# Kernel tuning notes

Measured on AMD Instinct MI355X. Metric: run time of the kernel, lower is better.

Reference implementation:

```python
import jax, jax.numpy as jnp
import numpy as np

OUT_F, IN_F = 11008, 4096
GROUP_SIZE = 128
NUM_GROUPS = IN_F // GROUP_SIZE  # 32


def setup_inputs() -> dict:
    key = jax.random.key(0)
    k1, k2, k3, k4 = jax.random.split(key, 4)
    x = jax.random.normal(k1, (2, 2048, IN_F), dtype=jnp.float32)
    # signed 4-bit RTN codes in [-8, 7]
    qweight = jax.random.randint(k2, (OUT_F, IN_F), 0, 16, dtype=jnp.int32) - 8
    # per-group scales (out_features, in_features // group_size)
    scales = jax.random.uniform(k3, (OUT_F, NUM_GROUPS), dtype=jnp.float32) * 0.02 + 1e-3
    bias = jax.random.normal(k4, (OUT_F,), dtype=jnp.float32) * 0.01
    return {"x": x, "qweight": qweight, "scales": scales, "bias": bias}


def reference(x, qweight, scales, bias):
    # RTN dequant: w[o, i] = qweight[o, i] * scales[o, i // group_size]
    w = (qweight.astype(x.dtype).reshape(OUT_F, NUM_GROUPS, GROUP_SIZE)
         * scales[:, :, None]).reshape(OUT_F, IN_F)
    # y = x @ w.T + bias  -> [batch, seq, out_features]
    return jnp.einsum('bsi,oi->bso', x, w) + bias
```

## Files before the change

### kernel.cpp

```cpp
#include <hip/hip_runtime.h>

#define OUT_F 11008
#define IN_F  4096
#define M_TOT 4096
#define BM    256
#define BN    256
#define BK    64
#define NKT   (IN_F / BK)
#define TM_N  (M_TOT / BM)
#define TN_N  (OUT_F / BN)
#define NWG   (TM_N * TN_N)

typedef __bf16 bf16;
typedef __attribute__((ext_vector_type(8))) __bf16 bf16x8;
typedef __attribute__((ext_vector_type(4))) float  floatx4;

#define GLD_LDS16(g, l) __builtin_amdgcn_global_load_lds(                      \
    (const __attribute__((address_space(1))) unsigned int*)(g),                \
    (__attribute__((address_space(3))) unsigned int*)(l), 16, 0, 0)

__global__ __launch_bounds__(256) void dequant_w_kernel(
    const int* __restrict__ qw, const float* __restrict__ sc,
    bf16* __restrict__ w) {
  const int idx  = blockIdx.x * 256 + threadIdx.x;
  const int o    = idx >> 9;
  const int iv   = idx & 511;
  const float s  = sc[o * (IN_F / 128) + (iv >> 4)];
  const int base = idx * 8;
  const int4* p  = (const int4*)(qw + base);
  const int4 q0  = p[0];
  const int4 q1  = p[1];
  bf16x8 v;
  v[0] = (bf16)((float)q0.x * s);
  v[1] = (bf16)((float)q0.y * s);
  v[2] = (bf16)((float)q0.z * s);
  v[3] = (bf16)((float)q0.w * s);
  v[4] = (bf16)((float)q1.x * s);
  v[5] = (bf16)((float)q1.y * s);
  v[6] = (bf16)((float)q1.z * s);
  v[7] = (bf16)((float)q1.w * s);
  *(bf16x8*)(w + base) = v;
}

__global__ __launch_bounds__(256) void cast_x_kernel(
    const float* __restrict__ x, bf16* __restrict__ xb) {
  const int idx  = blockIdx.x * 256 + threadIdx.x;
  const int base = idx * 8;
  const float4* p = (const float4*)(x + base);
  const float4 a = p[0];
  const float4 b = p[1];
  bf16x8 v;
  v[0] = (bf16)a.x; v[1] = (bf16)a.y; v[2] = (bf16)a.z; v[3] = (bf16)a.w;
  v[4] = (bf16)b.x; v[5] = (bf16)b.y; v[6] = (bf16)b.z; v[7] = (bf16)b.w;
  *(bf16x8*)(xb + base) = v;
}

__global__ __launch_bounds__(512, 2) void gemm_bt_bias_kernel(
    const bf16* __restrict__ A, const bf16* __restrict__ B,
    const float* __restrict__ bias, float* __restrict__ C) {
  __shared__ bf16 As[2][2][128 * 64];
  __shared__ bf16 Bs[2][2][128 * 64];

  const int t    = threadIdx.x;
  const int lane = t & 63;
  const int wv   = t >> 6;
  const int wm   = wv >> 2;
  const int wn   = wv & 3;
  const int lr   = lane & 15;
  const int lq   = lane >> 4;

  const int bid = blockIdx.x;
  const int swz = (bid & 7) * (NWG / 8) + (bid >> 3);
  const int bm  = (swz % TM_N) * BM;
  const int bn  = (swz / TM_N) * BN;

  const int sr  = t >> 3;
  const int sc  = t & 7;
  const int scx = (sc ^ (sr & 7)) * 8;
  const bf16* aStg = A + (bm + sr) * IN_F + scx;
  const bf16* bStg = B + (bn + sr) * IN_F + scx;

  auto stageA = [&](int buf, int h, int kt) {
    const bf16* g = aStg + h * 128 * IN_F + kt * BK;
    bf16* l = &As[buf][h][t * 8];
    GLD_LDS16(g, l);
    GLD_LDS16(g + 64 * IN_F, l + 4096);
  };
  auto stageB = [&](int buf, int h, int kt) {
    const bf16* g = bStg + h * 128 * IN_F + kt * BK;
    bf16* l = &Bs[buf][h][t * 8];
    GLD_LDS16(g, l);
    GLD_LDS16(g + 64 * IN_F, l + 4096);
  };

  const int xsw = (lr & 7) << 4;
  const int c0b = (lq * 16) ^ xsw;
  const int e0  = c0b >> 1;
  const int e1  = (c0b ^ 64) >> 1;

  floatx4 acc[8][4];
#pragma unroll
  for (int i = 0; i < 8; i++)
#pragma unroll
    for (int j = 0; j < 4; j++)
      acc[i][j] = (floatx4){0.f, 0.f, 0.f, 0.f};

  stageA(0, 0, 0); stageA(0, 1, 0); stageB(0, 0, 0); stageB(0, 1, 0);
  stageB(1, 0, 1); stageB(1, 1, 1);
  asm volatile("s_waitcnt vmcnt(4)" ::: "memory");
  __builtin_amdgcn_s_barrier();

  bf16x8 bfr[4][2];
  for (int kt = 0; kt < NKT; ++kt) {
    const int cur = kt & 1;
#pragma unroll
    for (int p = 0; p < 4; ++p) {
      bf16x8 af[2][2];
      const bf16* aBase = &As[cur][wm][0];
#pragma unroll
      for (int ii = 0; ii < 2; ++ii) {
        const int row = (2 * p + ii) * 16 + lr;
        af[ii][0] = *(const bf16x8*)&aBase[row * 64 + e0];
        af[ii][1] = *(const bf16x8*)&aBase[row * 64 + e1];
      }
      if (p == 0) {
        const bf16* bBase = &Bs[cur][wn >> 1][(wn & 1) * (64 * 64)];
#pragma unroll
        for (int j = 0; j < 4; ++j) {
          const int row = j * 16 + lr;
          bfr[j][0] = *(const bf16x8*)&bBase[row * 64 + e0];
          bfr[j][1] = *(const bf16x8*)&bBase[row * 64 + e1];
        }
      }

      if      (p == 0) { if (kt + 1 < NKT) stageA(cur ^ 1, 0, kt + 1); }
      else if (p == 1) { if (kt + 1 < NKT) stageA(cur ^ 1, 1, kt + 1); }
      else if (p == 2) { if (kt + 2 < NKT) stageB(cur, 0, kt + 2); }
      else             { if (kt + 2 < NKT) stageB(cur, 1, kt + 2); }

      __builtin_amdgcn_s_barrier();
      asm volatile("s_waitcnt lgkmcnt(0)" ::: "memory");
      __builtin_amdgcn_s_setprio(1);
#pragma unroll
      for (int ii = 0; ii < 2; ++ii)
#pragma unroll
        for (int j = 0; j < 4; ++j)
#pragma unroll
          for (int kk = 0; kk < 2; ++kk)
            acc[2 * p + ii][j] = __builtin_amdgcn_mfma_f32_16x16x32_bf16(
                af[ii][kk], bfr[j][kk], acc[2 * p + ii][j], 0, 0, 0);
      __builtin_amdgcn_s_setprio(0);
      if (p == 3) {
        if (kt + 2 < NKT) {
          asm volatile("s_waitcnt vmcnt(4)" ::: "memory");
        } else {
          asm volatile("s_waitcnt vmcnt(0)" ::: "memory");
        }
      }
      __builtin_amdgcn_s_barrier();
    }
  }

#pragma unroll
  for (int j = 0; j < 4; ++j) {
    const int col = bn + wn * 64 + j * 16 + lr;
    const float bv = bias[col];
#pragma unroll
    for (int i = 0; i < 8; ++i) {
      const int row0 = bm + wm * 128 + i * 16 + lq * 4;
#pragma unroll
      for (int r = 0; r < 4; ++r)
        __builtin_nontemporal_store(
            acc[i][j][r] + bv, &C[(size_t)(row0 + r) * OUT_F + col]);
    }
  }
}

extern "C" void kernel_launch(void* const* d_in, const int* in_sizes, int n_in,
                              void* d_out, int out_size, void* d_ws, size_t ws_size,
                              hipStream_t stream) {
  const float* x    = (const float*)d_in[0];
  const int*   qw   = (const int*)d_in[1];
  const float* sc   = (const float*)d_in[2];
  const float* bias = (const float*)d_in[3];
  float* out = (float*)d_out;

  bf16* wq = (bf16*)d_ws;
  bf16* xb = (bf16*)((char*)d_ws + (size_t)OUT_F * IN_F * sizeof(bf16));

  dequant_w_kernel<<<(OUT_F * IN_F / 8) / 256, 256, 0, stream>>>(qw, sc, wq);
  cast_x_kernel<<<(M_TOT * IN_F / 8) / 256, 256, 0, stream>>>(x, xb);

  gemm_bt_bias_kernel<<<dim3(NWG), 512, 0, stream>>>(xb, wq, bias, out);
}
```

Before: 838.3 us.

## Double-buffer A fragments in registers to overlap LDS reads with MFMA

Restructures the GEMM main loop so each phase reads the next A fragment from LDS into a second register set while MFMAs run on the previous one. B fragments and the first A fragment of the next K-tile are prefetched after the last phase's MFMAs. The explicit lgkmcnt(0) wait before each MFMA block is gone, and the loop is unrolled by two K-tiles via macros. The aim is to hide LDS read latency behind matrix-core work. The cost is higher register pressure and a more fragile barrier and waitcnt schedule.

```diff
diff --git a/kernel.cpp b/kernel.cpp
--- a/kernel.cpp
+++ b/kernel.cpp
@@ -80,18 +80,14 @@
   const bf16* aStg = A + (bm + sr) * IN_F + scx;
   const bf16* bStg = B + (bn + sr) * IN_F + scx;
 
-  auto stageA = [&](int buf, int h, int kt) {
-    const bf16* g = aStg + h * 128 * IN_F + kt * BK;
-    bf16* l = &As[buf][h][t * 8];
-    GLD_LDS16(g, l);
-    GLD_LDS16(g + 64 * IN_F, l + 4096);
-  };
-  auto stageB = [&](int buf, int h, int kt) {
-    const bf16* g = bStg + h * 128 * IN_F + kt * BK;
-    bf16* l = &Bs[buf][h][t * 8];
-    GLD_LDS16(g, l);
-    GLD_LDS16(g + 64 * IN_F, l + 4096);
-  };
+#define STAGE_A(BUF, H, KT)                                                  \
+  { const bf16* g_ = aStg + (H) * 128 * IN_F + (KT) * BK;                    \
+    GLD_LDS16(g_, &As[BUF][H][t * 8]);                                       \
+    GLD_LDS16(g_ + 64 * IN_F, &As[BUF][H][t * 8 + 4096]); }
+#define STAGE_B(BUF, H, KT)                                                  \
+  { const bf16* g_ = bStg + (H) * 128 * IN_F + (KT) * BK;                    \
+    GLD_LDS16(g_, &Bs[BUF][H][t * 8]);                                       \
+    GLD_LDS16(g_ + 64 * IN_F, &Bs[BUF][H][t * 8 + 4096]); }
 
   const int xsw = (lr & 7) << 4;
   const int c0b = (lq * 16) ^ xsw;
@@ -105,60 +101,75 @@
     for (int j = 0; j < 4; j++)
       acc[i][j] = (floatx4){0.f, 0.f, 0.f, 0.f};
 
-  stageA(0, 0, 0); stageA(0, 1, 0); stageB(0, 0, 0); stageB(0, 1, 0);
-  stageB(1, 0, 1); stageB(1, 1, 1);
+  bf16x8 afA[2][2], afB[2][2], bfr[4][2];
+
+#define READ_AF(DST, CURB, I0)                                               \
+  { const bf16* aB_ = &As[CURB][wm][0];                                      \
+    _Pragma("unroll") for (int ii_ = 0; ii_ < 2; ++ii_) {                    \
+      const int row_ = ((I0) + ii_) * 16 + lr;                               \
+      DST[ii_][0] = *(const bf16x8*)&aB_[row_ * 64 + e0];                    \
+      DST[ii_][1] = *(const bf16x8*)&aB_[row_ * 64 + e1]; } }
+
+#define READ_BF(CURB)                                                        \
+  { const bf16* bB_ = &Bs[CURB][wn >> 1][(wn & 1) * (64 * 64)];              \
+    _Pragma("unroll") for (int j_ = 0; j_ < 4; ++j_) {                       \
+      const int row_ = j_ * 16 + lr;                                         \
+      bfr[j_][0] = *(const bf16x8*)&bB_[row_ * 64 + e0];                     \
+      bfr[j_][1] = *(const bf16x8*)&bB_[row_ * 64 + e1]; } }
+
+#define MFMA_PH(AFS, I0)                                                     \
+  __builtin_amdgcn_s_setprio(1);                                             \
+  _Pragma("unroll") for (int ii_ = 0; ii_ < 2; ++ii_)                        \
+    _Pragma("unroll") for (int j_ = 0; j_ < 4; ++j_)                         \
+      _Pragma("unroll") for (int kk_ = 0; kk_ < 2; ++kk_)                    \
+        acc[(I0) + ii_][j_] = __builtin_amdgcn_mfma_f32_16x16x32_bf16(       \
+            AFS[ii_][kk_], bfr[j_][kk_], acc[(I0) + ii_][j_], 0, 0, 0);      \
+  __builtin_amdgcn_s_setprio(0);
+
+  STAGE_A(0, 0, 0) STAGE_A(0, 1, 0) STAGE_B(0, 0, 0) STAGE_B(0, 1, 0)
+  STAGE_B(1, 0, 1) STAGE_B(1, 1, 1)
   asm volatile("s_waitcnt vmcnt(4)" ::: "memory");
   __builtin_amdgcn_s_barrier();
-
-  bf16x8 bfr[4][2];
-  for (int kt = 0; kt < NKT; ++kt) {
-    const int cur = kt & 1;
-#pragma unroll
-    for (int p = 0; p < 4; ++p) {
-      bf16x8 af[2][2];
-      const bf16* aBase = &As[cur][wm][0];
-#pragma unroll
-      for (int ii = 0; ii < 2; ++ii) {
-        const int row = (2 * p + ii) * 16 + lr;
-        af[ii][0] = *(const bf16x8*)&aBase[row * 64 + e0];
-        af[ii][1] = *(const bf16x8*)&aBase[row * 64 + e1];
-      }
-      if (p == 0) {
-        const bf16* bBase = &Bs[cur][wn >> 1][(wn & 1) * (64 * 64)];
-#pragma unroll
-        for (int j = 0; j < 4; ++j) {
-          const int row = j * 16 + lr;
-          bfr[j][0] = *(const bf16x8*)&bBase[row * 64 + e0];
-          bfr[j][1] = *(const bf16x8*)&bBase[row * 64 + e1];
-        }
-      }
-
-      if      (p == 0) { if (kt + 1 < NKT) stageA(cur ^ 1, 0, kt + 1); }
-      else if (p == 1) { if (kt + 1 < NKT) stageA(cur ^ 1, 1, kt + 1); }
-      else if (p == 2) { if (kt + 2 < NKT) stageB(cur, 0, kt + 2); }
-      else             { if (kt + 2 < NKT) stageB(cur, 1, kt + 2); }
-
-      __builtin_amdgcn_s_barrier();
-      asm volatile("s_waitcnt lgkmcnt(0)" ::: "memory");
-      __builtin_amdgcn_s_setprio(1);
-#pragma unroll
-      for (int ii = 0; ii < 2; ++ii)
-#pragma unroll
-        for (int j = 0; j < 4; ++j)
-#pragma unroll
-          for (int kk = 0; kk < 2; ++kk)
-            acc[2 * p + ii][j] = __builtin_amdgcn_mfma_f32_16x16x32_bf16(
-                af[ii][kk], bfr[j][kk], acc[2 * p + ii][j], 0, 0, 0);
-      __builtin_amdgcn_s_setprio(0);
-      if (p == 3) {
-        if (kt + 2 < NKT) {
-          asm volatile("s_waitcnt vmcnt(4)" ::: "memory");
-        } else {
-          asm volatile("s_waitcnt vmcnt(0)" ::: "memory");
-        }
-      }
-      __builtin_amdgcn_s_barrier();
-    }
+  READ_AF(afA, 0, 0)
+  READ_BF(0)
+
+  for (int ktb = 0; ktb < NKT; ktb += 2) {
+#define TILE_BODY(CUR, NXT, KT)                                              \
+    { const int kt_ = (KT);                                                  \
+       \
+      READ_AF(afB, CUR, 2)                                                   \
+      if (kt_ + 1 < NKT) STAGE_A(NXT, 0, kt_ + 1)                            \
+      __builtin_amdgcn_s_barrier();                                          \
+      MFMA_PH(afA, 0)                                                        \
+      __builtin_amdgcn_s_barrier();                                          \
+       \
+      READ_AF(afA, CUR, 4)                                                   \
+      if (kt_ + 1 < NKT) STAGE_A(NXT, 1, kt_ + 1)                            \
+      __builtin_amdgcn_s_barrier();                                          \
+      MFMA_PH(afB, 2)                                                        \
+      __builtin_amdgcn_s_barrier();                                          \
+       \
+      READ_AF(afB, CUR, 6)                                                   \
+      if (kt_ + 2 < NKT) STAGE_B(CUR, 0, kt_ + 2)                            \
+      __builtin_amdgcn_s_barrier();                                          \
+      MFMA_PH(afA, 4)                                                        \
+      __builtin_amdgcn_s_barrier();                                          \
+         \
+         \
+      if (kt_ + 2 < NKT) {                                                   \
+        STAGE_B(CUR, 1, kt_ + 2)                                             \
+        asm volatile("s_waitcnt vmcnt(4)" ::: "memory");                     \
+      } else {                                                               \
+        asm volatile("s_waitcnt vmcnt(0)" ::: "memory");                     \
+      }                                                                      \
+      __builtin_amdgcn_s_barrier();                                          \
+      if (kt_ + 1 < NKT) READ_AF(afA, NXT, 0)                                \
+      MFMA_PH(afB, 6)                                                        \
+      if (kt_ + 1 < NKT) READ_BF(NXT)                                        \
+      __builtin_amdgcn_s_barrier(); }
+    TILE_BODY(0, 1, ktb)
+    TILE_BODY(1, 0, ktb + 1)
+#undef TILE_BODY
   }
 
 #pragma unroll
```

Result: faster. 769.1 us (-8.3%).
